# Optimization experiments

Hardware: AMD Instinct MI355X
Metric: run time of the kernel (lower is better)

The kernel has to match this reference:

```python
import jax, jax.numpy as jnp
import numpy as np

EMBED_DIM = 768
FF_DIM = 3072
NUM_EXPERTS = 8
TOP_K = 2
CAPACITY_FACTOR = 1.25  # training-mode capacity factor
LB_WEIGHT = 0.01
Z_WEIGHT = 0.001


def setup_inputs() -> dict:
    key = jax.random.key(0)
    k0, k1, k2, k3, k4 = jax.random.split(key, 5)
    B, S, D, F, E = 4, 2048, EMBED_DIM, FF_DIM, NUM_EXPERTS
    scale_d = 1.0 / np.sqrt(D)
    scale_f = 1.0 / np.sqrt(F)
    return {
        "x": jax.random.normal(k0, (B, S, D), dtype=jnp.float32),
        # router gate: nn.Linear(D, E, bias=False) -> weight [E, D]
        "w_gate": jax.random.normal(k1, (E, D), dtype=jnp.float32) * scale_d,
        # stacked expert weights, torch Linear layout [out, in]
        "wi_gate": jax.random.normal(k2, (E, F, D), dtype=jnp.float32) * scale_d,
        "wi_up": jax.random.normal(k3, (E, F, D), dtype=jnp.float32) * scale_d,
        "wo": jax.random.normal(k4, (E, D, F), dtype=jnp.float32) * scale_f,
    }


def moe_forward(x, w_gate, wi_gate, wi_up, wo):
    B, S, D = x.shape
    E = w_gate.shape[0]
    K = TOP_K
    T = B * S
    capacity = max(int(T * K / E * CAPACITY_FACTOR), K)

    xf = x.reshape(T, D)
    router_logits = xf @ w_gate.T                        # [T, E]
    router_probs = jax.nn.softmax(router_logits, axis=-1)
    topk_probs, topk_idx = jax.lax.top_k(router_probs, K)  # [T, K]
    topk_probs = topk_probs / topk_probs.sum(axis=-1, keepdims=True)

    # one-hot dispatch mask [T, K, E]
    onehot = (topk_idx[:, :, None] == jnp.arange(E)[None, None, :]).astype(xf.dtype)
    # per-(k, expert) arrival rank of each token (torch truncates first `capacity`
    # tokens in token-index order, independently per k and per expert)
    rank = ((jnp.cumsum(onehot, axis=0) - onehot) * onehot).sum(-1)  # [T, K]
    keep = (rank < capacity).astype(xf.dtype)                        # [T, K]

    # combine weights per (token, expert) [T, E]
    combine = jnp.einsum('tk,tk,tke->te', topk_probs, keep, onehot)

    out = jnp.zeros_like(xf)
    for e in range(E):  # fixed small structural loop over experts
        gate = jax.nn.silu(xf @ wi_gate[e].T)   # [T, F]
        up = xf @ wi_up[e].T                    # [T, F]
        y = (gate * up) @ wo[e].T               # [T, D]
        out = out + y * combine[:, e:e + 1]

    # auxiliary losses
    expert_mask = onehot.sum(axis=1)            # [T, E]
    f = expert_mask.sum(axis=0) / (T * K)
    P = router_probs.mean(axis=0)
    load_balance_loss = E * (f * P).sum()
    z_loss = jnp.mean(jax.nn.logsumexp(router_logits, axis=-1) ** 2)
    aux_loss = LB_WEIGHT * load_balance_loss + Z_WEIGHT * z_loss

    return out.reshape(B, S, D), aux_loss


def reference(x, w_gate, wi_gate, wi_up, wo):
    return moe_forward(x, w_gate, wi_gate, wi_up, wo)
```

## Files before the change

kernel.cpp:

```cpp
#include <hip/hip_runtime.h>

typedef unsigned short u16;
typedef unsigned int u32;
typedef unsigned long long u64;

#define T_TOK 8192
#define DIM 768
#define FF 3072
#define NE 8
#define CAP 2560
#define LSTR 5120
#define MAXMT 20
#define NCAST 27648

typedef __attribute__((ext_vector_type(8))) short s8v;
typedef __attribute__((ext_vector_type(4))) float f4v;

__device__ __forceinline__ u16 f2bf(float f) {
  union { float f; u32 u; } v; v.f = f;
  u32 r = v.u + 0x7FFFu + ((v.u >> 16) & 1u);
  return (u16)(r >> 16);
}

__device__ __forceinline__ void glds16(const void* g, void* l) {
  __builtin_amdgcn_global_load_lds(
      (const __attribute__((address_space(1))) u32*)g,
      (__attribute__((address_space(3))) u32*)l, 16, 0, 0);
}

__global__ __launch_bounds__(256) void pre_kernel(
    const float* __restrict__ wig, const float* __restrict__ wiu, const float* __restrict__ wo,
    u16* __restrict__ wgb, u16* __restrict__ wub, u16* __restrict__ wob, int n8each,
    const float* __restrict__ x, const float* __restrict__ wg, u16* __restrict__ xb,
    int* __restrict__ tki, float* __restrict__ tkp,
    float* __restrict__ probs, float* __restrict__ lse2) {
  int bid = blockIdx.x;
  if (bid < NCAST) {
    int i = bid * 256 + threadIdx.x;
    const float* s; u16* d; int j;
    if (i < n8each) { s = wig; d = wgb; j = i; }
    else if (i < 2 * n8each) { s = wiu; d = wub; j = i - n8each; }
    else { s = wo; d = wob; j = i - 2 * n8each; }
    const float4* s4 = (const float4*)s;
    float4 a = s4[2 * j], b = s4[2 * j + 1];
    uint4 o;
    o.x = (u32)f2bf(a.x) | ((u32)f2bf(a.y) << 16);
    o.y = (u32)f2bf(a.z) | ((u32)f2bf(a.w) << 16);
    o.z = (u32)f2bf(b.x) | ((u32)f2bf(b.y) << 16);
    o.w = (u32)f2bf(b.z) | ((u32)f2bf(b.w) << 16);
    ((uint4*)d)[j] = o;
    return;
  }
  int rb = bid - NCAST;
  int lane = threadIdx.x & 63;
  int t = rb * 4 + (threadIdx.x >> 6);
  const float* xr = x + (long)t * DIM;
  u16* xw = xb + (long)t * DIM;
  float acc[NE];
#pragma unroll
  for (int e = 0; e < NE; e++) acc[e] = 0.f;
  for (int i = 0; i < DIM / 64; i++) {
    float xv = xr[lane + 64 * i];
    xw[lane + 64 * i] = f2bf(xv);
#pragma unroll
    for (int e = 0; e < NE; e++) acc[e] += xv * wg[e * DIM + lane + 64 * i];
  }
#pragma unroll
  for (int off = 32; off > 0; off >>= 1) {
#pragma unroll
    for (int e = 0; e < NE; e++) acc[e] += __shfl_xor(acc[e], off);
  }
  if (lane == 0) {
    float m = acc[0];
#pragma unroll
    for (int e = 1; e < NE; e++) m = fmaxf(m, acc[e]);
    float p[NE], s = 0.f;
#pragma unroll
    for (int e = 0; e < NE; e++) { p[e] = __expf(acc[e] - m); s += p[e]; }
    float inv = 1.f / s;
    int e0 = 0;
#pragma unroll
    for (int e = 1; e < NE; e++) if (acc[e] > acc[e0]) e0 = e;
    int e1 = (e0 == 0) ? 1 : 0;
#pragma unroll
    for (int e = 0; e < NE; e++) if (e != e0 && acc[e] > acc[e1]) e1 = e;
    float p0 = p[e0] * inv, p1 = p[e1] * inv;
    float rn = 1.f / (p0 + p1);
    tki[2 * t] = e0; tki[2 * t + 1] = e1;
    tkp[2 * t] = p0 * rn; tkp[2 * t + 1] = p1 * rn;
    float4 pa = {p[0] * inv, p[1] * inv, p[2] * inv, p[3] * inv};
    float4 pb = {p[4] * inv, p[5] * inv, p[6] * inv, p[7] * inv};
    ((float4*)(probs + t * 8))[0] = pa;
    ((float4*)(probs + t * 8))[1] = pb;
    float lse = __logf(s) + m;
    lse2[t] = lse * lse;
  }
}

__global__ __launch_bounds__(1024) void reduce_router_kernel(
    const int* __restrict__ tki, const float* __restrict__ probs, const float* __restrict__ lse2,
    int* __restrict__ fcnt, float* __restrict__ psum, float* __restrict__ zsum) {
  int t = blockIdx.x * 1024 + threadIdx.x;
  float4 pa = ((const float4*)(probs + t * 8))[0];
  float4 pb = ((const float4*)(probs + t * 8))[1];
  float p[8] = {pa.x, pa.y, pa.z, pa.w, pb.x, pb.y, pb.z, pb.w};
  float z = lse2[t];
  int e0 = tki[2 * t], e1 = tki[2 * t + 1];
  int fc[8];
#pragma unroll
  for (int e = 0; e < 8; e++) fc[e] = (e0 == e ? 1 : 0) + (e1 == e ? 1 : 0);
#pragma unroll
  for (int off = 32; off > 0; off >>= 1) {
#pragma unroll
    for (int e = 0; e < 8; e++) { p[e] += __shfl_xor(p[e], off); fc[e] += __shfl_xor(fc[e], off); }
    z += __shfl_xor(z, off);
  }
  __shared__ float sp[16][9];
  __shared__ int sf[16][8];
  int wv = threadIdx.x >> 6, lane = threadIdx.x & 63;
  if (lane == 0) {
#pragma unroll
    for (int e = 0; e < 8; e++) { sp[wv][e] = p[e]; sf[wv][e] = fc[e]; }
    sp[wv][8] = z;
  }
  __syncthreads();
  if (threadIdx.x < 9) {
    float s = 0.f;
    for (int w = 0; w < 16; w++) s += sp[w][threadIdx.x];
    if (threadIdx.x < 8) atomicAdd(&psum[threadIdx.x], s);
    else atomicAdd(zsum, s);
  }
  if (threadIdx.x >= 64 && threadIdx.x < 72) {
    int e = threadIdx.x - 64;
    int s = 0;
    for (int w = 0; w < 16; w++) s += sf[w][e];
    atomicAdd(&fcnt[e], s);
  }
}

__global__ __launch_bounds__(1024) void rank_dispatch_kernel(
    const int* __restrict__ tki, const float* __restrict__ tkp,
    int* __restrict__ ltk, float* __restrict__ lw,
    int* __restrict__ counts, int* __restrict__ baserow, int* __restrict__ kflags) {
  __shared__ int wave_cnt[2][16][8];
  __shared__ int base[2][8];
  __shared__ int sc0[8];
  int tid = threadIdx.x, wv = tid >> 6, lane = tid & 63;
  int c0w[8];
#pragma unroll
  for (int e = 0; e < 8; e++) c0w[e] = 0;
  for (int c = 0; c < T_TOK / 1024; c++) {
    int e0 = tki[2 * (c * 1024 + tid)];
#pragma unroll
    for (int e = 0; e < 8; e++) {
      u64 m = __ballot(e0 == e);
      if (lane == 0) c0w[e] += __popcll(m);
    }
  }
  if (lane == 0) {
#pragma unroll
    for (int e = 0; e < 8; e++) wave_cnt[0][wv][e] = c0w[e];
  }
  if (tid < 16) base[tid >> 3][tid & 7] = 0;
  __syncthreads();
  if (tid < 8) {
    int s = 0;
    for (int w = 0; w < 16; w++) s += wave_cnt[0][w][tid];
    sc0[tid] = (s < CAP) ? s : CAP;
  }
  __syncthreads();
  u64 lmask = (lane == 63) ? 0x7FFFFFFFFFFFFFFFull : ((1ull << lane) - 1ull);
  for (int c = 0; c < T_TOK / 1024; c++) {
    int t = c * 1024 + tid;
    int e0 = tki[2 * t], e1 = tki[2 * t + 1];
    float p0 = tkp[2 * t], p1 = tkp[2 * t + 1];
    int pre0 = 0, pre1 = 0;
    for (int e = 0; e < 8; e++) {
      u64 m0 = __ballot(e0 == e);
      if (e0 == e) pre0 = __popcll(m0 & lmask);
      if (lane == 0) wave_cnt[0][wv][e] = __popcll(m0);
      u64 m1 = __ballot(e1 == e);
      if (e1 == e) pre1 = __popcll(m1 & lmask);
      if (lane == 0) wave_cnt[1][wv][e] = __popcll(m1);
    }
    __syncthreads();
    if (tid < 16) {
      int k = tid >> 3, e = tid & 7;
      int run = base[k][e];
      for (int w = 0; w < 16; w++) {
        int v = wave_cnt[k][w][e];
        wave_cnt[k][w][e] = run;
        run += v;
      }
      base[k][e] = run;
    }
    __syncthreads();
    int r0 = wave_cnt[0][wv][e0] + pre0;
    int r1 = wave_cnt[1][wv][e1] + pre1;
    if (r0 < CAP) { ltk[e0 * LSTR + r0] = (t << 1); lw[e0 * LSTR + r0] = p0; }
    if (r1 < CAP) {
      int p = sc0[e1] + r1;
      ltk[e1 * LSTR + p] = (t << 1) | 1; lw[e1 * LSTR + p] = p1;
    }
    kflags[t] = (r0 < CAP ? 1 : 0) | (r1 < CAP ? 2 : 0);
    __syncthreads();
  }
  if (tid == 0) {
    int run = 0;
    for (int e = 0; e < 8; e++) {
      int c1 = base[1][e]; if (c1 > CAP) c1 = CAP;
      int cnt = sc0[e] + c1;
      counts[e] = cnt; baserow[e] = run; run += cnt;
    }
  }
}

__global__ __launch_bounds__(256, 2) void gemm1_kernel(
    const u16* __restrict__ xb, const u16* __restrict__ wgb, const u16* __restrict__ wub,
    u16* __restrict__ H, const int* __restrict__ counts, const int* __restrict__ baserow,
    const int* __restrict__ ltk) {
  int id = blockIdx.x;
  int xcd = id & 7;
  int q = id >> 3;
  int gg = q / MAXMT;
  int mt = q - gg * MAXMT;
  int g = gg * 8 + xcd;
  int e = g / 48;
  int nt = g - e * 48;
  int cnt = counts[e];
  if (mt * 128 >= cnt) return;

  __shared__ u16 As[128 * 64];
  __shared__ u16 Bg[64 * 64];
  __shared__ u16 Bu[64 * 64];
  __shared__ int toks[128];
  int tid = threadIdx.x;
  if (tid < 128) {
    int r = mt * 128 + tid; if (r > cnt - 1) r = cnt - 1;
    toks[tid] = ltk[e * LSTR + r] >> 1;
  }
  __syncthreads();
  int rq8 = tid >> 3;
  int swz = ((tid & 7) ^ (rq8 & 7)) * 8;
  long tA0 = toks[rq8], tA1 = toks[32 + rq8], tA2 = toks[64 + rq8], tA3 = toks[96 + rq8];
  const u16* gA0 = xb + tA0 * DIM + swz;
  const u16* gA1 = xb + tA1 * DIM + swz;
  const u16* gA2 = xb + tA2 * DIM + swz;
  const u16* gA3 = xb + tA3 * DIM + swz;
  long bO0 = ((long)e * FF + nt * 64 + rq8) * DIM + swz;
  long bO1 = bO0 + 32l * DIM;
  const u16* gG0 = wgb + bO0; const u16* gG1 = wgb + bO1;
  const u16* gU0 = wub + bO0; const u16* gU1 = wub + bO1;
  u16* dA0 = As + tid * 8; u16* dA1 = dA0 + 2048; u16* dA2 = dA0 + 4096; u16* dA3 = dA0 + 6144;
  u16* dG0 = Bg + tid * 8; u16* dG1 = dG0 + 2048;
  u16* dU0 = Bu + tid * 8; u16* dU1 = dU0 + 2048;

  int lane = tid & 63, wv = tid >> 6;
  int wm = (wv & 1) * 64, wn = (wv >> 1) * 32;
  int lrow = lane & 15, quad = lane >> 4;
  int sl0 = (quad ^ (lrow & 7)) * 8;
  int sl1 = ((quad + 4) ^ (lrow & 7)) * 8;

  f4v zero = {0.f, 0.f, 0.f, 0.f};
  f4v accg[4][2], accu[4][2];
#pragma unroll
  for (int i = 0; i < 4; i++)
#pragma unroll
    for (int j = 0; j < 2; j++) { accg[i][j] = zero; accu[i][j] = zero; }

  for (int kt = 0; kt < DIM / 64; kt++) {
    int ko = kt * 64;
    __syncthreads();
    glds16(gA0 + ko, dA0); glds16(gA1 + ko, dA1);
    glds16(gA2 + ko, dA2); glds16(gA3 + ko, dA3);
    glds16(gG0 + ko, dG0); glds16(gG1 + ko, dG1);
    glds16(gU0 + ko, dU0); glds16(gU1 + ko, dU1);
    __syncthreads();
#pragma unroll
    for (int kk = 0; kk < 2; kk++) {
      int sl = kk ? sl1 : sl0;
      s8v a[4], bgf[2], buf[2];
#pragma unroll
      for (int i = 0; i < 4; i++)
        a[i] = *(const s8v*)&As[(wm + i * 16 + lrow) * 64 + sl];
#pragma unroll
      for (int j = 0; j < 2; j++) {
        bgf[j] = *(const s8v*)&Bg[(wn + j * 16 + lrow) * 64 + sl];
        buf[j] = *(const s8v*)&Bu[(wn + j * 16 + lrow) * 64 + sl];
      }
#pragma unroll
      for (int i = 0; i < 4; i++)
#pragma unroll
        for (int j = 0; j < 2; j++) {
          accg[i][j] = __builtin_amdgcn_mfma_f32_16x16x32_bf16(a[i], bgf[j], accg[i][j], 0, 0, 0);
          accu[i][j] = __builtin_amdgcn_mfma_f32_16x16x32_bf16(a[i], buf[j], accu[i][j], 0, 0, 0);
        }
    }
  }
  long hb = (long)baserow[e] + (long)mt * 128;
#pragma unroll
  for (int i = 0; i < 4; i++) {
#pragma unroll
    for (int r = 0; r < 4; r++) {
      int m = wm + i * 16 + quad * 4 + r;
      if (mt * 128 + m < cnt) {
#pragma unroll
        for (int j = 0; j < 2; j++) {
          float gv = accg[i][j][r], uv = accu[i][j][r];
          float h = gv / (1.f + __expf(-gv)) * uv;
          H[(hb + m) * FF + nt * 64 + wn + j * 16 + lrow] = f2bf(h);
        }
      }
    }
  }
}

__global__ __launch_bounds__(256, 2) void gemm2_kernel(
    const u16* __restrict__ H, const u16* __restrict__ wob,
    float* __restrict__ ybuf, const int* __restrict__ counts, const int* __restrict__ baserow,
    const int* __restrict__ ltk, const float* __restrict__ lw) {
  int id = blockIdx.x;
  int xcd = id & 7;
  int q = id >> 3;
  int gg = q / 6;
  int nt = q - gg * 6;
  int g = gg * 8 + xcd;
  int e = g / MAXMT;
  int mt = g - e * MAXMT;
  int cnt = counts[e];
  if (mt * 128 >= cnt) return;

  __shared__ u16 As[128 * 64];
  __shared__ u16 Bs[128 * 64];
  __shared__ int stok[128];
  __shared__ float sw[128];
  int tid = threadIdx.x;
  if (tid < 128) {
    int r = mt * 128 + tid; if (r > cnt - 1) r = cnt - 1;
    stok[tid] = ltk[e * LSTR + r];
    sw[tid] = lw[e * LSTR + r];
  }
  long hb = (long)baserow[e] + (long)mt * 128;
  int rq8 = tid >> 3;
  int swz = ((tid & 7) ^ (rq8 & 7)) * 8;
  const u16* gA0 = H + (hb + rq8) * FF + swz;
  const u16* gA1 = gA0 + 32l * FF;
  const u16* gA2 = gA0 + 64l * FF;
  const u16* gA3 = gA0 + 96l * FF;
  long bOff = ((long)e * DIM + nt * 128 + rq8) * FF + swz;
  const u16* gB0 = wob + bOff;
  const u16* gB1 = gB0 + 32l * FF;
  const u16* gB2 = gB0 + 64l * FF;
  const u16* gB3 = gB0 + 96l * FF;
  u16* dA0 = As + tid * 8; u16* dA1 = dA0 + 2048; u16* dA2 = dA0 + 4096; u16* dA3 = dA0 + 6144;
  u16* dB0 = Bs + tid * 8; u16* dB1 = dB0 + 2048; u16* dB2 = dB0 + 4096; u16* dB3 = dB0 + 6144;
  int lane = tid & 63, wv = tid >> 6;
  int wm = (wv & 1) * 64, wn = (wv >> 1) * 64;
  int lrow = lane & 15, quad = lane >> 4;
  int sl0 = (quad ^ (lrow & 7)) * 8;
  int sl1 = ((quad + 4) ^ (lrow & 7)) * 8;
  f4v zero = {0.f, 0.f, 0.f, 0.f};
  f4v acc[4][4];
#pragma unroll
  for (int i = 0; i < 4; i++)
#pragma unroll
    for (int j = 0; j < 4; j++) acc[i][j] = zero;

  for (int kt = 0; kt < FF / 64; kt++) {
    int ko = kt * 64;
    __syncthreads();
    glds16(gA0 + ko, dA0); glds16(gA1 + ko, dA1);
    glds16(gA2 + ko, dA2); glds16(gA3 + ko, dA3);
    glds16(gB0 + ko, dB0); glds16(gB1 + ko, dB1);
    glds16(gB2 + ko, dB2); glds16(gB3 + ko, dB3);
    __syncthreads();
#pragma unroll
    for (int kk = 0; kk < 2; kk++) {
      int sl = kk ? sl1 : sl0;
      s8v a[4], b[4];
#pragma unroll
      for (int i = 0; i < 4; i++)
        a[i] = *(const s8v*)&As[(wm + i * 16 + lrow) * 64 + sl];
#pragma unroll
      for (int j = 0; j < 4; j++)
        b[j] = *(const s8v*)&Bs[(wn + j * 16 + lrow) * 64 + sl];
#pragma unroll
      for (int i = 0; i < 4; i++)
#pragma unroll
        for (int j = 0; j < 4; j++)
          acc[i][j] = __builtin_amdgcn_mfma_f32_16x16x32_bf16(a[i], b[j], acc[i][j], 0, 0, 0);
    }
  }
#pragma unroll
  for (int i = 0; i < 4; i++) {
#pragma unroll
    for (int r = 0; r < 4; r++) {
      int m = wm + i * 16 + quad * 4 + r;
      if (mt * 128 + m < cnt) {
        int entry = stok[m];
        float w = sw[m];
        long ob = (long)entry * DIM + nt * 128;
#pragma unroll
        for (int j = 0; j < 4; j++)
          ybuf[ob + wn + j * 16 + lrow] = acc[i][j][r] * w;
      }
    }
  }
}

__global__ __launch_bounds__(256) void combine_kernel(
    const float* __restrict__ ybuf, const int* __restrict__ kflags, float* __restrict__ out) {
  int idx = blockIdx.x * 256 + threadIdx.x;
  int t = idx / (DIM / 4);
  int d4 = idx - t * (DIM / 4);
  int kf = kflags[t];
  float4 r = {0.f, 0.f, 0.f, 0.f};
  if (kf & 1) {
    float4 a = ((const float4*)(ybuf + (long)(2 * t) * DIM))[d4];
    r.x += a.x; r.y += a.y; r.z += a.z; r.w += a.w;
  }
  if (kf & 2) {
    float4 b = ((const float4*)(ybuf + (long)(2 * t + 1) * DIM))[d4];
    r.x += b.x; r.y += b.y; r.z += b.z; r.w += b.w;
  }
  ((float4*)out)[idx] = r;
}

__global__ void aux_kernel(const int* __restrict__ fcnt, const float* __restrict__ psum,
                           const float* __restrict__ zsum, float* __restrict__ outaux) {
  if (threadIdx.x == 0 && blockIdx.x == 0) {
    float lb = 0.f;
    for (int e = 0; e < 8; e++)
      lb += ((float)fcnt[e] / (float)(T_TOK * 2)) * (psum[e] / (float)T_TOK);
    lb *= 8.f;
    float z = zsum[0] / (float)T_TOK;
    outaux[0] = 0.01f * lb + 0.001f * z;
  }
}

extern "C" void kernel_launch(void* const* d_in, const int* in_sizes, int n_in,
                              void* d_out, int out_size, void* d_ws, size_t ws_size,
                              hipStream_t stream) {
  const float* x = (const float*)d_in[0];
  const float* wgate = (const float*)d_in[1];
  const float* wig = (const float*)d_in[2];
  const float* wiu = (const float*)d_in[3];
  const float* wo = (const float*)d_in[4];
  float* out = (float*)d_out;

  char* ws = (char*)d_ws;
  size_t off = 0;
  auto alloc = [&](size_t bytes) {
    void* p = ws + off;
    off += (bytes + 255) & ~(size_t)255;
    return p;
  };
  int* ctrl = (int*)alloc(256);
  u16* xb = (u16*)alloc((size_t)T_TOK * DIM * 2);
  u16* wgb = (u16*)alloc((size_t)NE * FF * DIM * 2);
  u16* wub = (u16*)alloc((size_t)NE * FF * DIM * 2);
  u16* wob = (u16*)alloc((size_t)NE * DIM * FF * 2);
  u16* Hbuf = (u16*)alloc((size_t)(T_TOK * 2 + 128) * FF * 2);
  int* tki = (int*)alloc((size_t)T_TOK * 2 * 4);
  float* tkp = (float*)alloc((size_t)T_TOK * 2 * 4);
  int* ltk = (int*)alloc((size_t)NE * LSTR * 4);
  float* lw = (float*)alloc((size_t)NE * LSTR * 4);
  float* probs = (float*)alloc((size_t)T_TOK * 8 * 4);
  float* lse2 = (float*)alloc((size_t)T_TOK * 4);
  int* kflags = (int*)alloc((size_t)T_TOK * 4);
  float* ybuf = (float*)wgb;

  int* fcnt = ctrl;
  int* counts = ctrl + 8;
  int* baserow = ctrl + 16;
  float* psum = (float*)(ctrl + 24);
  float* zsum = (float*)(ctrl + 32);

  const int n8each = NE * FF * DIM / 8;
  hipMemsetAsync(ctrl, 0, 256, stream);
  pre_kernel<<<NCAST + T_TOK / 4, 256, 0, stream>>>(
      wig, wiu, wo, wgb, wub, wob, n8each, x, wgate, xb, tki, tkp, probs, lse2);
  reduce_router_kernel<<<T_TOK / 1024, 1024, 0, stream>>>(tki, probs, lse2, fcnt, psum, zsum);
  rank_dispatch_kernel<<<1, 1024, 0, stream>>>(tki, tkp, ltk, lw, counts, baserow, kflags);
  gemm1_kernel<<<8 * 48 * MAXMT, 256, 0, stream>>>(xb, wgb, wub, Hbuf, counts, baserow, ltk);
  gemm2_kernel<<<8 * MAXMT * 6, 256, 0, stream>>>(Hbuf, wob, ybuf, counts, baserow, ltk, lw);
  combine_kernel<<<T_TOK * DIM / 4 / 256, 256, 0, stream>>>(ybuf, kflags, out);
  aux_kernel<<<1, 64, 0, stream>>>(fcnt, psum, zsum, out + (size_t)T_TOK * DIM);
}
```

Before: 577.5 us.

## Overlap wo weight cast with rank dispatch and fold small kernels together

The wo fp32-to-bf16 cast moves out of pre_kernel into extra blocks of a merged kernel. That kernel also runs the single-block rank/dispatch work and the router reductions, so the cast fills the GPU while the serial one-block dispatch runs. The memset of the control buffer is folded into pre_kernel, and the aux-loss computation becomes an extra block of the combine kernel. This removes three launches and the idle time around the one-block kernel. In exchange, rank dispatch now shares its launch with thousands of cast blocks and may be scheduled later.

```diff
diff --git a/kernel.cpp b/kernel.cpp
--- a/kernel.cpp
+++ b/kernel.cpp
@@ -11,7 +11,9 @@
 #define CAP 2560
 #define LSTR 5120
 #define MAXMT 20
-#define NCAST 27648
+#define N8EACH 2359296
+#define NCAST2 18432
+#define NWOCAST 2304
 
 typedef __attribute__((ext_vector_type(8))) short s8v;
 typedef __attribute__((ext_vector_type(4))) float f4v;
@@ -28,30 +30,32 @@
       (__attribute__((address_space(3))) u32*)l, 16, 0, 0);
 }
 
+__device__ __forceinline__ void cast8(const float* __restrict__ s, u16* __restrict__ d, int j) {
+  const float4* s4 = (const float4*)s;
+  float4 a = s4[2 * j], b = s4[2 * j + 1];
+  uint4 o;
+  o.x = (u32)f2bf(a.x) | ((u32)f2bf(a.y) << 16);
+  o.y = (u32)f2bf(a.z) | ((u32)f2bf(a.w) << 16);
+  o.z = (u32)f2bf(b.x) | ((u32)f2bf(b.y) << 16);
+  o.w = (u32)f2bf(b.z) | ((u32)f2bf(b.w) << 16);
+  ((uint4*)d)[j] = o;
+}
+
 __global__ __launch_bounds__(256) void pre_kernel(
-    const float* __restrict__ wig, const float* __restrict__ wiu, const float* __restrict__ wo,
-    u16* __restrict__ wgb, u16* __restrict__ wub, u16* __restrict__ wob, int n8each,
+    const float* __restrict__ wig, const float* __restrict__ wiu,
+    u16* __restrict__ wgb, u16* __restrict__ wub,
     const float* __restrict__ x, const float* __restrict__ wg, u16* __restrict__ xb,
     int* __restrict__ tki, float* __restrict__ tkp,
-    float* __restrict__ probs, float* __restrict__ lse2) {
+    float* __restrict__ probs, float* __restrict__ lse2, int* __restrict__ ctrl) {
   int bid = blockIdx.x;
-  if (bid < NCAST) {
+  if (bid == 0 && threadIdx.x < 64) ctrl[threadIdx.x] = 0;
+  if (bid < NCAST2) {
     int i = bid * 256 + threadIdx.x;
-    const float* s; u16* d; int j;
-    if (i < n8each) { s = wig; d = wgb; j = i; }
-    else if (i < 2 * n8each) { s = wiu; d = wub; j = i - n8each; }
-    else { s = wo; d = wob; j = i - 2 * n8each; }
-    const float4* s4 = (const float4*)s;
-    float4 a = s4[2 * j], b = s4[2 * j + 1];
-    uint4 o;
-    o.x = (u32)f2bf(a.x) | ((u32)f2bf(a.y) << 16);
-    o.y = (u32)f2bf(a.z) | ((u32)f2bf(a.w) << 16);
-    o.z = (u32)f2bf(b.x) | ((u32)f2bf(b.y) << 16);
-    o.w = (u32)f2bf(b.z) | ((u32)f2bf(b.w) << 16);
-    ((uint4*)d)[j] = o;
+    if (i < N8EACH) cast8(wig, wgb, i);
+    else cast8(wiu, wub, i - N8EACH);
     return;
   }
-  int rb = bid - NCAST;
+  int rb = bid - NCAST2;
   int lane = threadIdx.x & 63;
   int t = rb * 4 + (threadIdx.x >> 6);
   const float* xr = x + (long)t * DIM;
@@ -97,55 +101,63 @@
   }
 }
 
-__global__ __launch_bounds__(1024) void reduce_router_kernel(
-    const int* __restrict__ tki, const float* __restrict__ probs, const float* __restrict__ lse2,
-    int* __restrict__ fcnt, float* __restrict__ psum, float* __restrict__ zsum) {
-  int t = blockIdx.x * 1024 + threadIdx.x;
-  float4 pa = ((const float4*)(probs + t * 8))[0];
-  float4 pb = ((const float4*)(probs + t * 8))[1];
-  float p[8] = {pa.x, pa.y, pa.z, pa.w, pb.x, pb.y, pb.z, pb.w};
-  float z = lse2[t];
-  int e0 = tki[2 * t], e1 = tki[2 * t + 1];
-  int fc[8];
-#pragma unroll
-  for (int e = 0; e < 8; e++) fc[e] = (e0 == e ? 1 : 0) + (e1 == e ? 1 : 0);
-#pragma unroll
-  for (int off = 32; off > 0; off >>= 1) {
-#pragma unroll
-    for (int e = 0; e < 8; e++) { p[e] += __shfl_xor(p[e], off); fc[e] += __shfl_xor(fc[e], off); }
-    z += __shfl_xor(z, off);
-  }
-  __shared__ float sp[16][9];
-  __shared__ int sf[16][8];
-  int wv = threadIdx.x >> 6, lane = threadIdx.x & 63;
-  if (lane == 0) {
-#pragma unroll
-    for (int e = 0; e < 8; e++) { sp[wv][e] = p[e]; sf[wv][e] = fc[e]; }
-    sp[wv][8] = z;
-  }
-  __syncthreads();
-  if (threadIdx.x < 9) {
-    float s = 0.f;
-    for (int w = 0; w < 16; w++) s += sp[w][threadIdx.x];
-    if (threadIdx.x < 8) atomicAdd(&psum[threadIdx.x], s);
-    else atomicAdd(zsum, s);
-  }
-  if (threadIdx.x >= 64 && threadIdx.x < 72) {
-    int e = threadIdx.x - 64;
-    int s = 0;
-    for (int w = 0; w < 16; w++) s += sf[w][e];
-    atomicAdd(&fcnt[e], s);
-  }
-}
-
-__global__ __launch_bounds__(1024) void rank_dispatch_kernel(
+__global__ __launch_bounds__(1024) void rankred_kernel(
     const int* __restrict__ tki, const float* __restrict__ tkp,
+    const float* __restrict__ probs, const float* __restrict__ lse2,
     int* __restrict__ ltk, float* __restrict__ lw,
-    int* __restrict__ counts, int* __restrict__ baserow, int* __restrict__ kflags) {
+    int* __restrict__ counts, int* __restrict__ baserow, int* __restrict__ kflags,
+    int* __restrict__ fcnt, float* __restrict__ psum, float* __restrict__ zsum,
+    const float* __restrict__ wo, u16* __restrict__ wob) {
+  int bid = blockIdx.x;
+  int tid = threadIdx.x;
+  if (bid >= 9) {
+    int j = (bid - 9) * 1024 + tid;
+    cast8(wo, wob, j);
+    return;
+  }
+  if (bid >= 1) {
+    int t = (bid - 1) * 1024 + tid;
+    float4 pa = ((const float4*)(probs + t * 8))[0];
+    float4 pb = ((const float4*)(probs + t * 8))[1];
+    float p[8] = {pa.x, pa.y, pa.z, pa.w, pb.x, pb.y, pb.z, pb.w};
+    float z = lse2[t];
+    int e0 = tki[2 * t], e1 = tki[2 * t + 1];
+    int fc[8];
+#pragma unroll
+    for (int e = 0; e < 8; e++) fc[e] = (e0 == e ? 1 : 0) + (e1 == e ? 1 : 0);
+#pragma unroll
+    for (int off = 32; off > 0; off >>= 1) {
+#pragma unroll
+      for (int e = 0; e < 8; e++) { p[e] += __shfl_xor(p[e], off); fc[e] += __shfl_xor(fc[e], off); }
+      z += __shfl_xor(z, off);
+    }
+    __shared__ float sp[16][9];
+    __shared__ int sf[16][8];
+    int wv = tid >> 6, lane = tid & 63;
+    if (lane == 0) {
+#pragma unroll
+      for (int e = 0; e < 8; e++) { sp[wv][e] = p[e]; sf[wv][e] = fc[e]; }
+      sp[wv][8] = z;
+    }
+    __syncthreads();
+    if (tid < 9) {
+      float s = 0.f;
+      for (int w = 0; w < 16; w++) s += sp[w][tid];
+      if (tid < 8) atomicAdd(&psum[tid], s);
+      else atomicAdd(zsum, s);
+    }
+    if (tid >= 64 && tid < 72) {
+      int e = tid - 64;
+      int s = 0;
+      for (int w = 0; w < 16; w++) s += sf[w][e];
+      atomicAdd(&fcnt[e], s);
+    }
+    return;
+  }
   __shared__ int wave_cnt[2][16][8];
   __shared__ int base[2][8];
   __shared__ int sc0[8];
-  int tid = threadIdx.x, wv = tid >> 6, lane = tid & 63;
+  int wv = tid >> 6, lane = tid & 63;
   int c0w[8];
 #pragma unroll
   for (int e = 0; e < 8; e++) c0w[e] = 0;
@@ -408,9 +420,22 @@
   }
 }
 
-__global__ __launch_bounds__(256) void combine_kernel(
-    const float* __restrict__ ybuf, const int* __restrict__ kflags, float* __restrict__ out) {
-  int idx = blockIdx.x * 256 + threadIdx.x;
+__global__ __launch_bounds__(256) void combine_aux_kernel(
+    const float* __restrict__ ybuf, const int* __restrict__ kflags, float* __restrict__ out,
+    const int* __restrict__ fcnt, const float* __restrict__ psum, const float* __restrict__ zsum) {
+  int bid = blockIdx.x;
+  if (bid == T_TOK * DIM / 4 / 256) {
+    if (threadIdx.x == 0) {
+      float lb = 0.f;
+      for (int e = 0; e < 8; e++)
+        lb += ((float)fcnt[e] / (float)(T_TOK * 2)) * (psum[e] / (float)T_TOK);
+      lb *= 8.f;
+      float z = zsum[0] / (float)T_TOK;
+      out[(size_t)T_TOK * DIM] = 0.01f * lb + 0.001f * z;
+    }
+    return;
+  }
+  int idx = bid * 256 + threadIdx.x;
   int t = idx / (DIM / 4);
   int d4 = idx - t * (DIM / 4);
   int kf = kflags[t];
@@ -424,18 +449,6 @@
     r.x += b.x; r.y += b.y; r.z += b.z; r.w += b.w;
   }
   ((float4*)out)[idx] = r;
-}
-
-__global__ void aux_kernel(const int* __restrict__ fcnt, const float* __restrict__ psum,
-                           const float* __restrict__ zsum, float* __restrict__ outaux) {
-  if (threadIdx.x == 0 && blockIdx.x == 0) {
-    float lb = 0.f;
-    for (int e = 0; e < 8; e++)
-      lb += ((float)fcnt[e] / (float)(T_TOK * 2)) * (psum[e] / (float)T_TOK);
-    lb *= 8.f;
-    float z = zsum[0] / (float)T_TOK;
-    outaux[0] = 0.01f * lb + 0.001f * z;
-  }
 }
 
 extern "C" void kernel_launch(void* const* d_in, const int* in_sizes, int n_in,
@@ -476,14 +489,12 @@
   float* psum = (float*)(ctrl + 24);
   float* zsum = (float*)(ctrl + 32);
 
-  const int n8each = NE * FF * DIM / 8;
-  hipMemsetAsync(ctrl, 0, 256, stream);
-  pre_kernel<<<NCAST + T_TOK / 4, 256, 0, stream>>>(
-      wig, wiu, wo, wgb, wub, wob, n8each, x, wgate, xb, tki, tkp, probs, lse2);
-  reduce_router_kernel<<<T_TOK / 1024, 1024, 0, stream>>>(tki, probs, lse2, fcnt, psum, zsum);
-  rank_dispatch_kernel<<<1, 1024, 0, stream>>>(tki, tkp, ltk, lw, counts, baserow, kflags);
+  pre_kernel<<<NCAST2 + T_TOK / 4, 256, 0, stream>>>(
+      wig, wiu, wgb, wub, x, wgate, xb, tki, tkp, probs, lse2, ctrl);
+  rankred_kernel<<<9 + NWOCAST, 1024, 0, stream>>>(
+      tki, tkp, probs, lse2, ltk, lw, counts, baserow, kflags, fcnt, psum, zsum, wo, wob);
   gemm1_kernel<<<8 * 48 * MAXMT, 256, 0, stream>>>(xb, wgb, wub, Hbuf, counts, baserow, ltk);
   gemm2_kernel<<<8 * MAXMT * 6, 256, 0, stream>>>(Hbuf, wob, ybuf, counts, baserow, ltk, lw);
-  combine_kernel<<<T_TOK * DIM / 4 / 256, 256, 0, stream>>>(ybuf, kflags, out);
-  aux_kernel<<<1, 64, 0, stream>>>(fcnt, psum, zsum, out + (size_t)T_TOK * DIM);
-}
+  combine_aux_kernel<<<T_TOK * DIM / 4 / 256 + 1, 256, 0, stream>>>(
+      ybuf, kflags, out, fcnt, psum, zsum);
+}
```

Result: faster. 551.7 us (-4.5%).
